# Kernel tuning notes

Hardware: AMD Instinct MI355X
Metric: run time of the kernel (lower is better)

## Reference

```python
import jax, jax.numpy as jnp
import numpy as np

B, C, T = 16, 129, 2000
NF, ED, K = 40, 64, 16

def setup_inputs() -> dict:
    key = jax.random.key(0)
    ks = iter(jax.random.split(key, 48))
    def n(shape, s=0.05):
        return jax.random.normal(next(ks), shape, jnp.float32) * s
    inp = {
        'x': jax.random.normal(next(ks), (B, C, T), jnp.float32),
        # temporal conv (1,25) pad (0,12) + BN (inference running stats)
        'tconv_w': n((NF, 1, 1, 25)), 'tconv_b': jnp.zeros((NF,)),
        'tbn_g': jnp.ones((NF,)), 'tbn_b': jnp.zeros((NF,)), 'tbn_m': n((NF,)), 'tbn_v': jnp.ones((NF,)),
        # spatial conv (C,1) + BN
        'sconv_w': n((NF, NF, C, 1)), 'sconv_b': jnp.zeros((NF,)),
        'sbn_g': jnp.ones((NF,)), 'sbn_b': jnp.zeros((NF,)), 'sbn_m': n((NF,)), 'sbn_v': jnp.ones((NF,)),
        # separable: depthwise (1,15) pad (0,7), pointwise 1x1 -> 2*NF, BN
        'dw_w': n((NF, 1, 1, 15)), 'dw_b': jnp.zeros((NF,)),
        'pw_w': n((2 * NF, NF, 1, 1)), 'pw_b': jnp.zeros((2 * NF,)),
        'pbn_g': jnp.ones((2 * NF,)), 'pbn_b': jnp.zeros((2 * NF,)), 'pbn_m': n((2 * NF,)), 'pbn_v': jnp.ones((2 * NF,)),
        # projection 2*NF -> ED
        'proj_w': n((ED, 2 * NF)), 'proj_b': jnp.zeros((ED,)),
        # ENN cell 0 (input ED)
        'wx0': n((K, ED)), 'L0': jnp.eye(K, dtype=jnp.float32) + 0.1 * n((K, K), 1.0),
        'll0': jnp.asarray(np.log(0.1), jnp.float32), 'b0': jnp.zeros((K,)),
        'ln0_g': jnp.ones((K,)), 'ln0_b': jnp.zeros((K,)),
        # ENN cell 1 (input K)
        'wx1': n((K, K)), 'L1': jnp.eye(K, dtype=jnp.float32) + 0.1 * n((K, K), 1.0),
        'll1': jnp.asarray(np.log(0.1), jnp.float32), 'b1': jnp.zeros((K,)),
        'ln1_g': jnp.ones((K,)), 'ln1_b': jnp.zeros((K,)),
        # collapse
        'wq_w': n((K, K)), 'wq_b': jnp.zeros((K,)), 'log_temp': jnp.asarray(0.0, jnp.float32),
    }
    return inp

def _conv(x, w, b, pad, groups=1):
    y = jax.lax.conv_general_dilated(
        x, w, window_strides=(1, 1), padding=pad,
        dimension_numbers=('NCHW', 'OIHW', 'NCHW'), feature_group_count=groups)
    return y + b[None, :, None, None]

def _bn(x, g, b, m, v, eps=1e-5):
    inv = g / jnp.sqrt(v + eps)
    return x * inv[None, :, None, None] + (b - m * inv)[None, :, None, None]

def _cell(x, h, Wx, L, ll, b, g, be, eps=1e-5):
    E = L @ L.T  # PSD entanglement matrix [K,K]
    pre = x @ Wx.T + h @ E.T - jnp.exp(ll) * h + b
    mu = pre.mean(-1, keepdims=True)
    var = pre.var(-1, keepdims=True)
    pre = (pre - mu) / jnp.sqrt(var + eps) * g + be
    return jnp.tanh(pre)

def _forward(x, tconv_w, tconv_b, tbn_g, tbn_b, tbn_m, tbn_v,
             sconv_w, sconv_b, sbn_g, sbn_b, sbn_m, sbn_v,
             dw_w, dw_b, pw_w, pw_b, pbn_g, pbn_b, pbn_m, pbn_v,
             proj_w, proj_b,
             wx0, L0, ll0, b0, ln0_g, ln0_b,
             wx1, L1, ll1, b1, ln1_g, ln1_b,
             wq_w, wq_b, log_temp):
    # ---- SpatialCNN front-end (BN in inference mode, dropout=identity) ----
    o = x[:, None, :, :]                                        # [B,1,C,T]
    o = _conv(o, tconv_w, tconv_b, ((0, 0), (12, 12)))          # [B,NF,C,T]
    o = jax.nn.elu(_bn(o, tbn_g, tbn_b, tbn_m, tbn_v))
    o = _conv(o, sconv_w, sconv_b, ((0, 0), (0, 0)))            # [B,NF,1,T]
    o = jax.nn.elu(_bn(o, sbn_g, sbn_b, sbn_m, sbn_v))
    o = _conv(o, dw_w, dw_b, ((0, 0), (7, 7)), groups=NF)       # depthwise
    o = _conv(o, pw_w, pw_b, ((0, 0), (0, 0)))                  # [B,2NF,1,T]
    o = jax.nn.elu(_bn(o, pbn_g, pbn_b, pbn_m, pbn_v))
    Bn, Ch, _, Tt = o.shape
    o = o.reshape(Bn, Ch, Tt // 4, 4).mean(-1)                  # AvgPool (1,4) -> [B,2NF,T']
    feats = o.transpose(0, 2, 1) @ proj_w.T + proj_b            # [B,T',ED]
    # ---- Entangled RNN over T' steps (lax.scan) ----
    h_init = (jnp.zeros((Bn, K), feats.dtype), jnp.zeros((Bn, K), feats.dtype))
    def step(carry, xt):
        h0, h1 = carry
        h0 = _cell(xt, h0, wx0, L0, ll0, b0, ln0_g, ln0_b)
        h1 = _cell(h0, h1, wx1, L1, ll1, b1, ln1_g, ln1_b)
        return (h0, h1), None
    (h0, h1), _ = jax.lax.scan(step, h_init, feats.transpose(1, 0, 2))
    Z = h1                                                       # [B,K]
    # ---- Collapse attention ----
    q = Z @ wq_w.T + wq_b
    scores = jnp.sum(q * Z, axis=-1, keepdims=True)              # [B,1]
    alpha = jax.nn.softmax(scores / jnp.exp(log_temp), axis=-1)  # [B,1]
    return Z, alpha

def reference(x, tconv_w, tconv_b, tbn_g, tbn_b, tbn_m, tbn_v,
              sconv_w, sconv_b, sbn_g, sbn_b, sbn_m, sbn_v,
              dw_w, dw_b, pw_w, pw_b, pbn_g, pbn_b, pbn_m, pbn_v,
              proj_w, proj_b,
              wx0, L0, ll0, b0, ln0_g, ln0_b,
              wx1, L1, ll1, b1, ln1_g, ln1_b,
              wq_w, wq_b, log_temp):
    return _forward(x, tconv_w, tconv_b, tbn_g, tbn_b, tbn_m, tbn_v,
                    sconv_w, sconv_b, sbn_g, sbn_b, sbn_m, sbn_v,
                    dw_w, dw_b, pw_w, pw_b, pbn_g, pbn_b, pbn_m, pbn_v,
                    proj_w, proj_b,
                    wx0, L0, ll0, b0, ln0_g, ln0_b,
                    wx1, L1, ll1, b1, ln1_g, ln1_b,
                    wq_w, wq_b, log_temp)
```

## Files before the change

kernel.cpp:

```cpp
#include <hip/hip_runtime.h>
#include <math.h>

#define B_ 16
#define C_ 129
#define T_ 2000
#define NF_ 40
#define ED_ 64
#define K_ 16
#define TP_ 500

#define OFF_SB2 1040
#define OFF_PWC 1088
#define OFF_PB2 4288
#define OFF_WP  4368
#define OFF_BP  5648
#define OFF_M0  5664
#define OFF_M1  5920
#define OFF_W1A 6224
#define OFF_W2U 8192
#define OFF_XP  1495040
#define OFF_S2R 1623040

typedef __attribute__((ext_vector_type(8))) short s8v;
typedef __attribute__((ext_vector_type(4))) float f4v;

#define XROW 292

__device__ __forceinline__ float elu_f(float x) {
    return x > 0.f ? x : (__expf(x) - 1.f);
}
__device__ __forceinline__ float tanh2_f(float a2) {
    return fmaf(-2.f, __builtin_amdgcn_rcpf(__expf(a2) + 1.f), 1.f);
}
__device__ __forceinline__ unsigned bfr(float v) {
    return (__float_as_uint(v) + 0x8000u) >> 16;
}

#define DPPF(v, ctrl) __int_as_float(__builtin_amdgcn_update_dpp( \
    0, __float_as_int(v), (ctrl), 0xF, 0xF, false))
#define DPPI(v, ctrl) __builtin_amdgcn_update_dpp(0, (v), (ctrl), 0xF, 0xF, false)

#define RSUM16(s) do {                     \
    s += DPPF(s, 0x128);                   \
    s += DPPF(s, 0x124);                   \
    s += DPPF(s, 0x122);                   \
    s += DPPF(s, 0x121);                   \
} while (0)

struct P0 {
    const float *tconv_w, *tconv_b, *tbn_g, *tbn_b, *tbn_m, *tbn_v;
    const float *sconv_b, *sbn_g, *sbn_b, *sbn_m, *sbn_v;
    const float *pw_w, *pw_b, *pbn_g, *pbn_b, *pbn_m, *pbn_v;
    const float *proj_w, *proj_b, *wx0, *b0, *L0, *ll0, *L1, *ll1;
    const float *sconv_w;
    float* ws;
};

__global__ __launch_bounds__(256) void k0_all(P0 p) {
    const int tid = threadIdx.x;
    float* ws = p.ws;
    const float eps = 1e-5f;

    if (blockIdx.x < 1250) {
        const int i = blockIdx.x * 256 + tid;
        if (i < 320000)
            ((float4*)(ws + OFF_S2R))[i] = make_float4(0.f, 0.f, 0.f, 0.f);
        return;
    }
    if (blockIdx.x < 1444) {
        const int e = (blockIdx.x - 1250) * 256 + tid;
        if (e >= C_ * 3 * 2 * 64) return;
        unsigned short* w2b = (unsigned short*)(ws + OFF_W2U);
        const int c = e / 384;
        int r = e - c * 384;
        const int mt = r >> 7; r &= 127;
        const int kc = r >> 6;
        const int lane = r & 63;
        const int g = mt * 16 + (lane & 15);
        const float sinv = (g < NF_) ? p.sbn_g[g] * rsqrtf(p.sbn_v[g] + 1e-5f) : 0.f;
        unsigned short o[8];
#pragma unroll
        for (int j = 0; j < 8; ++j) {
            const int f = kc * 32 + (lane >> 4) * 8 + j;
            float v = 0.f;
            if (g < NF_ && f < NF_) v = p.sconv_w[g * (NF_ * C_) + f * C_ + c] * sinv;
            o[j] = (unsigned short)bfr(v);
        }
        unsigned short* dst = w2b + (size_t)e * 8;
#pragma unroll
        for (int j = 0; j < 8; ++j) dst[j] = o[j];
        return;
    }

    const int gtid = (blockIdx.x - 1444) * 256 + tid;
    const int stride = 8 * 256;
    for (int e = gtid; e < 192; e += stride) {
        const int mt = e >> 6, L = e & 63;
        const int f = mt * 16 + (L & 15);
        float inv = 0.f, bias = 0.f;
        if (f < NF_) {
            inv = p.tbn_g[f] / sqrtf(p.tbn_v[f] + eps);
            bias = p.tconv_b[f] * inv + p.tbn_b[f] - p.tbn_m[f] * inv;
        }
        unsigned short* dst = ((unsigned short*)(ws + OFF_W1A)) + e * 8;
#pragma unroll
        for (int j = 0; j < 8; ++j) {
            const int k = (L >> 4) * 8 + j;
            float v = 0.f;
            if (f < NF_) {
                if (k < 25) v = p.tconv_w[f * 25 + k] * inv;
                else if (k == 25) v = bias;
            }
            dst[j] = (unsigned short)bfr(v);
        }
    }
    for (int f = gtid; f < NF_; f += stride) {
        const float sinv = p.sbn_g[f] / sqrtf(p.sbn_v[f] + eps);
        ws[OFF_SB2 + f] = p.sconv_b[f] * sinv + p.sbn_b[f] - p.sbn_m[f] * sinv;
    }
    for (int e = gtid; e < 3200; e += stride) {
        const int g = e / 40;
        const float pinv = p.pbn_g[g] / sqrtf(p.pbn_v[g] + eps);
        ws[OFF_PWC + e] = p.pw_w[e] * pinv;
    }
    for (int g = gtid; g < 80; g += stride) {
        const float pinv = p.pbn_g[g] / sqrtf(p.pbn_v[g] + eps);
        ws[OFF_PB2 + g] = p.pw_b[g] * pinv + p.pbn_b[g] - p.pbn_m[g] * pinv;
    }
    for (int e = gtid; e < 1280; e += stride) {
        const int k = e / 80, g = e - k * 80;
        float a = 0.f;
        for (int ee = 0; ee < ED_; ++ee)
            a = fmaf(p.wx0[k * ED_ + ee], p.proj_w[ee * 80 + g], a);
        ws[OFF_WP + e] = a;
    }
    for (int k = gtid; k < K_; k += stride) {
        float a = p.b0[k];
        for (int ee = 0; ee < ED_; ++ee)
            a = fmaf(p.wx0[k * ED_ + ee], p.proj_b[ee], a);
        ws[OFF_BP + k] = a;
    }
    for (int e = gtid; e < 256; e += stride) {
        const int k = e >> 4, j = e & 15;
        float a0 = 0.f, a1 = 0.f;
        for (int i = 0; i < 16; ++i) {
            a0 = fmaf(p.L0[k * 16 + i], p.L0[j * 16 + i], a0);
            a1 = fmaf(p.L1[k * 16 + i], p.L1[j * 16 + i], a1);
        }
        if (k == j) { a0 -= expf(p.ll0[0]); a1 -= expf(p.ll1[0]); }
        ws[OFF_M0 + e] = a0;
        ws[OFF_M1 + e] = a1;
    }
}

__global__ __launch_bounds__(256, 4) void k1_mfma(
    const float* __restrict__ x, const unsigned short* __restrict__ w1a,
    const unsigned short* __restrict__ w2b, float* __restrict__ s2raw) {
    __shared__ float xs[17 * XROW];
    __shared__ unsigned int vsI[2048];

    const int tid = threadIdx.x;
    const int split = blockIdx.x & 7;
    const int tile = (blockIdx.x >> 3) & 7;
    const int b = blockIdx.x >> 6;
    const int c0 = (split * C_) >> 3;
    const int c1 = ((split + 1) * C_) >> 3;
    const int cc = c1 - c0;
    const int t0 = tile << 8;
    const int w = tid >> 6;
    const int lane = tid & 63;
    const int n = lane & 15;
    const int q = lane >> 4;
    const int qh = q >> 1;
    const int q1_2 = (q & 1) * 2;
    const bool q3 = (q == 3);
    const int wb = w << 9;
    const int w64 = w << 6;
    const int ln8 = n + q * 8;

    for (int i = tid; i < 2048; i += 256) vsI[i] = 0u;
    for (int e = tid; e < cc * XROW; e += 256) {
        const int cl = e / XROW;
        const int i = e - cl * XROW;
        const int t = t0 - 12 + i;
        float v = 0.f;
        if ((unsigned)t < (unsigned)T_) v = x[(b * C_ + c0 + cl) * T_ + t];
        xs[e] = v;
    }
    __syncthreads();

    const s8v* w1a8 = (const s8v*)w1a;
    s8v wA[3];
#pragma unroll
    for (int mt = 0; mt < 3; ++mt) wA[mt] = w1a8[mt * 64 + lane];

    f4v acc[4][3];
#pragma unroll
    for (int nt = 0; nt < 4; ++nt)
#pragma unroll
        for (int mt = 0; mt < 3; ++mt) acc[nt][mt] = (f4v)0.f;

    const s8v* w2b8 = (const s8v*)w2b;
    const f4v z4 = (f4v)0.f;

    for (int cl = 0; cl < cc; ++cl) {
        const int c = c0 + cl;
        s8v af[3][2];
#pragma unroll
        for (int mt = 0; mt < 3; ++mt)
#pragma unroll
            for (int kc = 0; kc < 2; ++kc)
                af[mt][kc] = w2b8[((c * 3 + mt) * 2 + kc) * 64 + lane];

        const float* xrow = &xs[cl * XROW + w64 + ln8];

#pragma unroll
        for (int nt = 0; nt < 4; ++nt) {
            float bx[8];
#pragma unroll
            for (int j = 0; j < 8; ++j) bx[j] = xrow[nt * 16 + j];
            if (q3) bx[1] = 1.0f;
            unsigned pw_[4];
#pragma unroll
            for (int jj = 0; jj < 4; ++jj)
                pw_[jj] = bfr(bx[2 * jj]) |
                    ((__float_as_uint(bx[2 * jj + 1]) + 0x8000u) & 0xFFFF0000u);
            const s8v bh = *(const s8v*)pw_;
#pragma unroll
            for (int mt = 0; mt < 3; ++mt) {
                const f4v vT = __builtin_amdgcn_mfma_f32_16x16x32_bf16(
                    wA[mt], bh, z4, 0, 0, 0);
                const float e0 = elu_f(vT[0]);
                const float e1 = elu_f(vT[1]);
                const float e2 = elu_f(vT[2]);
                const float e3 = elu_f(vT[3]);
                const unsigned lo = bfr(e0) |
                    ((__float_as_uint(e1) + 0x8000u) & 0xFFFF0000u);
                const unsigned hi = bfr(e2) |
                    ((__float_as_uint(e3) + 0x8000u) & 0xFFFF0000u);
                const int base = wb + ((2 * mt + qh) << 6) + (n << 2) + q1_2;
                vsI[base] = lo;
                vsI[base + 1] = hi;
            }
            __builtin_amdgcn_wave_barrier();
            const s8v b0 = *(const s8v*)&vsI[wb + (q << 6) + (n << 2)];
            const s8v b1 = *(const s8v*)&vsI[wb + ((4 + q) << 6) + (n << 2)];
#pragma unroll
            for (int mt = 0; mt < 3; ++mt) {
                acc[nt][mt] = __builtin_amdgcn_mfma_f32_16x16x32_bf16(
                    af[mt][0], b0, acc[nt][mt], 0, 0, 0);
                acc[nt][mt] = __builtin_amdgcn_mfma_f32_16x16x32_bf16(
                    af[mt][1], b1, acc[nt][mt], 0, 0, 0);
            }
            __builtin_amdgcn_wave_barrier();
        }
    }

#pragma unroll
    for (int nt = 0; nt < 4; ++nt) {
        const int t = t0 + w * 64 + nt * 16 + n;
        if (t >= T_) continue;
#pragma unroll
        for (int mt = 0; mt < 3; ++mt) {
#pragma unroll
            for (int r = 0; r < 4; ++r) {
                const int g = mt * 16 + q * 4 + r;
                if (g < NF_)
                    atomicAdd(&s2raw[(b * NF_ + g) * T_ + t], acc[nt][mt][r]);
            }
        }
    }
}

__global__ __launch_bounds__(256) void k2_dwpw(
    const float* __restrict__ s2raw, const float* __restrict__ sb2,
    const float* __restrict__ dw_w, const float* __restrict__ dw_b,
    const float* __restrict__ pwc, const float* __restrict__ pb2,
    const float* __restrict__ WP, const float* __restrict__ bp,
    float* __restrict__ xp) {
    __shared__ float st[NF_ * 114];
    __shared__ float dwo[NF_ * 100];
    __shared__ float dwwl[NF_ * 15];
    __shared__ float dwbl[NF_];
    __shared__ float pwcl[80 * 40];
    __shared__ float pb2l[80];
    __shared__ float WPl[K_ * 80];
    __shared__ float bpl[K_];
    __shared__ float po[80 * 25];
    const int tid = threadIdx.x;
    const int b = blockIdx.x / 20;
    const int tp0 = (blockIdx.x % 20) * 25;
    const int tbase = tp0 * 4 - 7;
    for (int e = tid; e < NF_ * 114; e += 256) {
        const int f = e / 114;
        const int i = e - f * 114;
        const int t = tbase + i;
        float v = 0.f;
        if ((unsigned)t < (unsigned)T_)
            v = elu_f(s2raw[(b * NF_ + f) * T_ + t] + sb2[f]);
        st[e] = v;
    }
    for (int e = tid; e < 600; e += 256) dwwl[e] = dw_w[e];
    for (int e = tid; e < 3200; e += 256) pwcl[e] = pwc[e];
    for (int e = tid; e < 1280; e += 256) WPl[e] = WP[e];
    if (tid < NF_) dwbl[tid] = dw_b[tid];
    if (tid < 80) pb2l[tid] = pb2[tid];
    if (tid < K_) bpl[tid] = bp[tid];
    __syncthreads();
    for (int e = tid; e < 4000; e += 256) {
        const int f = e / 100;
        const int tq = e - f * 100;
        float a = dwbl[f];
#pragma unroll
        for (int kk = 0; kk < 15; ++kk)
            a = fmaf(dwwl[f * 15 + kk], st[f * 114 + tq + kk], a);
        dwo[e] = a;
    }
    __syncthreads();
    for (int e = tid; e < 2000; e += 256) {
        const int g = e / 25;
        const int tp = e - g * 25;
        float sum = 0.f;
#pragma unroll
        for (int dt = 0; dt < 4; ++dt) {
            float a = pb2l[g];
            for (int f = 0; f < NF_; ++f)
                a = fmaf(pwcl[g * 40 + f], dwo[f * 100 + tp * 4 + dt], a);
            sum += elu_f(a);
        }
        po[e] = sum * 0.25f;
    }
    __syncthreads();
    for (int e = tid; e < 400; e += 256) {
        const int tp = e >> 4;
        const int k = e & 15;
        float a = bpl[k];
        for (int g = 0; g < 80; ++g)
            a = fmaf(WPl[k * 80 + g], po[g * 25 + tp], a);
        xp[(b * TP_ + tp0 + tp) * K_ + k] = a;
    }
}

__global__ __launch_bounds__(64, 1) void k3_scan(
    const float* __restrict__ xp, const float* __restrict__ M0,
    const float* __restrict__ M1, const float* __restrict__ wx1,
    const float* __restrict__ b1, const float* __restrict__ ln0_g,
    const float* __restrict__ ln0_b, const float* __restrict__ ln1_g,
    const float* __restrict__ ln1_b, float* __restrict__ out) {
    const int lane = threadIdx.x;
    const int k = lane & 15;
    const int r = lane >> 4;
    const int b = blockIdx.x;

    float wrow[16];
    {
        int pid = k;
#pragma unroll
        for (int j = 0; j < 16; ++j) {
            pid = DPPI(pid, 0x121);
            const float w0 = M0[k * 16 + pid];
            const float w1v = wx1[k * 16 + pid];
            const float w2 = M1[k * 16 + pid];
            wrow[j] = (r == 0) ? w0 : (r == 1) ? w1v : (r == 2) ? w2 : 0.f;
        }
    }
    const float b1r = b1[k];
    const float g0 = 2.f * ln0_g[k], be0 = 2.f * ln0_b[k];
    const float g1 = 2.f * ln1_g[k], be1 = 2.f * ln1_b[k];
    const float* xpb = xp + b * TP_ * K_ + k;

    float h0c;
    {
        float x0 = xpb[0];
        float s1 = x0, s2 = x0 * x0;
        RSUM16(s1);
        RSUM16(s2);
        const float mu = s1 * 0.0625f;
        const float var = s2 * 0.0625f - mu * mu;
        const float rr = rsqrtf(var + 1e-5f);
        h0c = tanh2_f(fmaf((x0 - mu) * rr, g0, be0));
    }
    float h1c = 0.f;

    float xn[4];
    xn[1] = xpb[1 * K_];
    xn[2] = xpb[2 * K_];
    xn[3] = xpb[3 * K_];
    xn[0] = xpb[4 * K_];

    for (int t = 0; t < TP_; ++t) {
        float hr = (r == 2) ? h1c : h0c;
        float a0 = 0.f, a1 = 0.f;
#pragma unroll
        for (int j = 0; j < 16; j += 2) {
            hr = DPPF(hr, 0x121);
            a0 = fmaf(wrow[j], hr, a0);
            hr = DPPF(hr, 0x121);
            a1 = fmaf(wrow[j + 1], hr, a1);
        }
        const float acc = a0 + a1;

        const int slot = (t + 1) & 3;
        const float xv = xn[slot];
        int tf = t + 5;
        if (tf > TP_ - 1) tf = TP_ - 1;
        xn[slot] = xpb[tf * K_];

        const float A0 = __shfl(acc, k, 64);
        const float A1 = __shfl(acc, 16 + k, 64);
        const float A2 = __shfl(acc, 32 + k, 64);
        const float pre0 = A0 + xv;
        const float pre1 = (A1 + A2) + b1r;

        float s1 = pre0, s2 = pre0 * pre0;
        float u1 = pre1, u2 = pre1 * pre1;
        RSUM16(s1);
        RSUM16(s2);
        RSUM16(u1);
        RSUM16(u2);
        const float mu0 = s1 * 0.0625f;
        const float var0 = fmaf(s2, 0.0625f, -mu0 * mu0);
        const float r0 = rsqrtf(var0 + 1e-5f);
        const float mu1 = u1 * 0.0625f;
        const float var1 = fmaf(u2, 0.0625f, -mu1 * mu1);
        const float r1 = rsqrtf(var1 + 1e-5f);
        const float h0n = tanh2_f(fmaf((pre0 - mu0) * r0, g0, be0));
        const float h1n = tanh2_f(fmaf((pre1 - mu1) * r1, g1, be1));

        h1c = h1n;
        h0c = h0n;
    }
    if (lane < 16) {
        out[b * K_ + k] = h1c;
        if (k == 0) out[256 + b] = 1.0f;
    }
}

extern "C" void kernel_launch(void* const* d_in, const int* in_sizes, int n_in,
                              void* d_out, int out_size, void* d_ws, size_t ws_size,
                              hipStream_t stream) {
    const float* x       = (const float*)d_in[0];
    const float* dw_w    = (const float*)d_in[13];
    const float* dw_b    = (const float*)d_in[14];
    const float* wx1     = (const float*)d_in[29];
    const float* b1      = (const float*)d_in[32];
    const float* ln0_g   = (const float*)d_in[27];
    const float* ln0_b   = (const float*)d_in[28];
    const float* ln1_g   = (const float*)d_in[33];
    const float* ln1_b   = (const float*)d_in[34];
    float* ws = (float*)d_ws;
    float* out = (float*)d_out;

    P0 p;
    p.tconv_w = (const float*)d_in[1]; p.tconv_b = (const float*)d_in[2];
    p.tbn_g = (const float*)d_in[3]; p.tbn_b = (const float*)d_in[4];
    p.tbn_m = (const float*)d_in[5]; p.tbn_v = (const float*)d_in[6];
    p.sconv_b = (const float*)d_in[8];
    p.sbn_g = (const float*)d_in[9]; p.sbn_b = (const float*)d_in[10];
    p.sbn_m = (const float*)d_in[11]; p.sbn_v = (const float*)d_in[12];
    p.pw_w = (const float*)d_in[15]; p.pw_b = (const float*)d_in[16];
    p.pbn_g = (const float*)d_in[17]; p.pbn_b = (const float*)d_in[18];
    p.pbn_m = (const float*)d_in[19]; p.pbn_v = (const float*)d_in[20];
    p.proj_w = (const float*)d_in[21]; p.proj_b = (const float*)d_in[22];
    p.wx0 = (const float*)d_in[23]; p.b0 = (const float*)d_in[26];
    p.L0 = (const float*)d_in[24]; p.ll0 = (const float*)d_in[25];
    p.L1 = (const float*)d_in[30]; p.ll1 = (const float*)d_in[31];
    p.sconv_w = (const float*)d_in[7];
    p.ws = ws;

    unsigned short* w2b = (unsigned short*)(ws + OFF_W2U);
    unsigned short* w1a = (unsigned short*)(ws + OFF_W1A);

    k0_all<<<dim3(1452), dim3(256), 0, stream>>>(p);
    k1_mfma<<<dim3(1024), dim3(256), 0, stream>>>(x, w1a, w2b, ws + OFF_S2R);
    k2_dwpw<<<dim3(320), dim3(256), 0, stream>>>(ws + OFF_S2R, ws + OFF_SB2,
                                                 dw_w, dw_b, ws + OFF_PWC,
                                                 ws + OFF_PB2, ws + OFF_WP, ws + OFF_BP,
                                                 ws + OFF_XP);
    k3_scan<<<dim3(16), dim3(64), 0, stream>>>(ws + OFF_XP, ws + OFF_M0, ws + OFF_M1,
                                               wx1, b1, ln0_g, ln0_b, ln1_g, ln1_b, out);
}
```

Before: 420.7 us.

## Skew ENN scan so cell 0 and cell 1 run on separate half-waves

Restructures the recurrent scan so the upper half-wave computes cell 0 while the lower half-wave computes cell 1 one step behind, pipelining the two cells. The old version needed three cross-lane shuffles and four 16-lane reductions per step; the new one needs one shuffle and two reductions per lane group, shortening the serial dependency chain per step. The loop is unrolled by four with static prefetch slots and runs 504 iterations to absorb the one-step skew, capturing h1 at step 500. The correctness of the skew, the masking at step 0 and the extra iterations past the end is subtle.

```diff
diff --git a/kernel.cpp b/kernel.cpp
--- a/kernel.cpp
+++ b/kernel.cpp
@@ -341,6 +341,34 @@
     }
 }
 
+#define SCAN_STEP(I, S) do {                                              \
+    float vB = h0cur;                                                     \
+    float a0 = 0.f, a1 = 0.f, c0 = 0.f, c1 = 0.f;                         \
+    _Pragma("unroll")                                                     \
+    for (int j = 0; j < 16; j += 2) {                                     \
+        vA = DPPF(vA, 0x121);  a0 = fmaf(W1[j], vA, a0);                  \
+        vB = DPPF(vB, 0x121);  c0 = fmaf(W2[j], vB, c0);                  \
+        vA = DPPF(vA, 0x121);  a1 = fmaf(W1[j + 1], vA, a1);              \
+        vB = DPPF(vB, 0x121);  c1 = fmaf(W2[j + 1], vB, c1);              \
+    }                                                                     \
+    const float xv = xn[S];                                               \
+    int tf = (I) + 5; if (tf > TP_ - 1) tf = TP_ - 1;                     \
+    xn[S] = xpb[tf * K_];                                                 \
+    const float cadd = lower ? b1r : xv;                                  \
+    const float pre = ((a0 + a1) + (c0 + c1)) + cadd;                     \
+    float s1 = pre, s2 = pre * pre;                                       \
+    RSUM16(s1);                                                           \
+    RSUM16(s2);                                                           \
+    const float mu = s1 * 0.0625f;                                        \
+    const float var = fmaf(s2, 0.0625f, -mu * mu);                        \
+    float hn = tanh2_f(fmaf((pre - mu) * rsqrtf(var + 1e-5f), gg, bb));   \
+    if ((I) == 0 && lower) hn = 0.f;                                      \
+    vA = hn;                                                              \
+    h0cur = h0pend;                                                       \
+    h0pend = __shfl(hn, 32 + k, 64);                                      \
+    if ((I) == 500) h1out = vA;                                           \
+} while (0)
+
 __global__ __launch_bounds__(64, 1) void k3_scan(
     const float* __restrict__ xp, const float* __restrict__ M0,
     const float* __restrict__ M1, const float* __restrict__ wx1,
@@ -349,89 +377,57 @@
     const float* __restrict__ ln1_b, float* __restrict__ out) {
     const int lane = threadIdx.x;
     const int k = lane & 15;
-    const int r = lane >> 4;
+    const bool lower = lane < 32;
     const int b = blockIdx.x;
 
-    float wrow[16];
+    float W1[16], W2[16];
     {
         int pid = k;
 #pragma unroll
         for (int j = 0; j < 16; ++j) {
             pid = DPPI(pid, 0x121);
-            const float w0 = M0[k * 16 + pid];
-            const float w1v = wx1[k * 16 + pid];
-            const float w2 = M1[k * 16 + pid];
-            wrow[j] = (r == 0) ? w0 : (r == 1) ? w1v : (r == 2) ? w2 : 0.f;
+            const float m0 = M0[k * 16 + pid];
+            const float m1 = M1[k * 16 + pid];
+            const float wx = wx1[k * 16 + pid];
+            W1[j] = lower ? m1 : m0;
+            W2[j] = lower ? wx : 0.f;
         }
     }
     const float b1r = b1[k];
     const float g0 = 2.f * ln0_g[k], be0 = 2.f * ln0_b[k];
-    const float g1 = 2.f * ln1_g[k], be1 = 2.f * ln1_b[k];
+    const float gg = lower ? 2.f * ln1_g[k] : g0;
+    const float bb = lower ? 2.f * ln1_b[k] : be0;
     const float* xpb = xp + b * TP_ * K_ + k;
 
-    float h0c;
+    float h0_0;
     {
-        float x0 = xpb[0];
+        const float x0 = xpb[0];
         float s1 = x0, s2 = x0 * x0;
         RSUM16(s1);
         RSUM16(s2);
         const float mu = s1 * 0.0625f;
-        const float var = s2 * 0.0625f - mu * mu;
-        const float rr = rsqrtf(var + 1e-5f);
-        h0c = tanh2_f(fmaf((x0 - mu) * rr, g0, be0));
-    }
-    float h1c = 0.f;
+        const float var = fmaf(s2, 0.0625f, -mu * mu);
+        h0_0 = tanh2_f(fmaf((x0 - mu) * rsqrtf(var + 1e-5f), g0, be0));
+    }
+    float vA = lower ? 0.f : h0_0;
+    float h0cur = 0.f;
+    float h0pend = h0_0;
+    float h1out = 0.f;
 
     float xn[4];
-    xn[1] = xpb[1 * K_];
-    xn[2] = xpb[2 * K_];
-    xn[3] = xpb[3 * K_];
-    xn[0] = xpb[4 * K_];
-
-    for (int t = 0; t < TP_; ++t) {
-        float hr = (r == 2) ? h1c : h0c;
-        float a0 = 0.f, a1 = 0.f;
-#pragma unroll
-        for (int j = 0; j < 16; j += 2) {
-            hr = DPPF(hr, 0x121);
-            a0 = fmaf(wrow[j], hr, a0);
-            hr = DPPF(hr, 0x121);
-            a1 = fmaf(wrow[j + 1], hr, a1);
-        }
-        const float acc = a0 + a1;
-
-        const int slot = (t + 1) & 3;
-        const float xv = xn[slot];
-        int tf = t + 5;
-        if (tf > TP_ - 1) tf = TP_ - 1;
-        xn[slot] = xpb[tf * K_];
-
-        const float A0 = __shfl(acc, k, 64);
-        const float A1 = __shfl(acc, 16 + k, 64);
-        const float A2 = __shfl(acc, 32 + k, 64);
-        const float pre0 = A0 + xv;
-        const float pre1 = (A1 + A2) + b1r;
-
-        float s1 = pre0, s2 = pre0 * pre0;
-        float u1 = pre1, u2 = pre1 * pre1;
-        RSUM16(s1);
-        RSUM16(s2);
-        RSUM16(u1);
-        RSUM16(u2);
-        const float mu0 = s1 * 0.0625f;
-        const float var0 = fmaf(s2, 0.0625f, -mu0 * mu0);
-        const float r0 = rsqrtf(var0 + 1e-5f);
-        const float mu1 = u1 * 0.0625f;
-        const float var1 = fmaf(u2, 0.0625f, -mu1 * mu1);
-        const float r1 = rsqrtf(var1 + 1e-5f);
-        const float h0n = tanh2_f(fmaf((pre0 - mu0) * r0, g0, be0));
-        const float h1n = tanh2_f(fmaf((pre1 - mu1) * r1, g1, be1));
-
-        h1c = h1n;
-        h0c = h0n;
+    xn[0] = xpb[1 * K_];
+    xn[1] = xpb[2 * K_];
+    xn[2] = xpb[3 * K_];
+    xn[3] = xpb[4 * K_];
+
+    for (int i = 0; i < 504; i += 4) {
+        SCAN_STEP(i + 0, 0);
+        SCAN_STEP(i + 1, 1);
+        SCAN_STEP(i + 2, 2);
+        SCAN_STEP(i + 3, 3);
     }
     if (lane < 16) {
-        out[b * K_ + k] = h1c;
+        out[b * K_ + k] = h1out;
         if (k == 0) out[256 + b] = 1.0f;
     }
 }
```

Result: faster. 368.7 us (-12.4%).
